# Kernel optimization log

Measured on AMD Instinct MI355X. Metric: run time of the kernel, lower is better.

Reference implementation:

```python
import jax, jax.numpy as jnp
import numpy as np

GAMMA = 1.0
EPS = 1e-8


def setup_inputs() -> dict:
    key = jax.random.key(0)
    k1, k2 = jax.random.split(key)
    inputs = jax.random.normal(k1, (16, 2048, 1024), dtype=jnp.float32)
    codebook = jax.random.normal(k2, (2048, 1024), dtype=jnp.float32)  # normal(1.0) init
    return {"inputs": inputs, "codebook": codebook}


def reference(inputs, codebook):
    # inputs: [B, T, D]; codebook: [K, D]
    features = jax.lax.stop_gradient(inputs)
    # similarity = sum over D of features[..., None, :] * codebook -> [B, T, K]
    similarity = jnp.einsum('btd,kd->btk', features, codebook)
    scores = jax.nn.softmax(similarity, axis=-1)  # [B, T, K]
    nn_idx = jnp.argmax(scores, axis=-1)  # [B, T]
    # one_hot(nn_idx) @ codebook == direct gather
    quantized = codebook[nn_idx]  # [B, T, D]
    quantized = quantized - jnp.mean(quantized, axis=-1, keepdims=True)
    quantized = quantized / jnp.linalg.norm(quantized, axis=-1, keepdims=True)
    # entropy loss
    flat = scores.reshape(-1, scores.shape[-1])  # [B*T, K]
    h_clust = -jnp.mean(jnp.sum(flat * jnp.log2(flat + EPS), axis=-1))
    diversity = jnp.mean(flat, axis=0)  # [K]
    h_diversity = -jnp.sum(diversity * jnp.log2(diversity + EPS))
    loss = h_clust - GAMMA * h_diversity
    quantization_loss = jnp.full(scores.shape, loss)  # [B, T, K], scalar broadcast
    # straight-through estimator
    quantized = inputs + jax.lax.stop_gradient(quantized - inputs)
    return (quantized, quantization_loss, nn_idx, codebook)
```

## Files before the change

kernel.cpp:

```cpp
#include <hip/hip_runtime.h>
#include <math.h>

#define M_TOTAL 32768
#define D_DIM   1024
#define K_DIM   2048

#define OUT0_OFF 0ULL
#define OUT1_OFF 33554432ULL
#define OUT2_OFF 100663296ULL
#define OUT3_OFF 100696064ULL

typedef _Float16 f16x4 __attribute__((ext_vector_type(4)));
typedef _Float16 f16x8 __attribute__((ext_vector_type(8)));
typedef float    f32x4 __attribute__((ext_vector_type(4)));

__device__ __forceinline__ void async_copy16(void* lds, const void* g) {
    __builtin_amdgcn_global_load_lds(
        (const __attribute__((address_space(1))) unsigned int*)g,
        (__attribute__((address_space(3))) unsigned int*)lds, 16, 0, 0);
}

__global__ __launch_bounds__(256) void convcb_kernel(const float* __restrict__ C,
                                                     _Float16* __restrict__ ch,
                                                     _Float16* __restrict__ cl) {
    const int i = blockIdx.x * 256 + threadIdx.x;
    const float4 c = ((const float4*)C)[i];
    f16x4 h, l;
    h.x = (_Float16)c.x; l.x = (_Float16)(c.x - (float)h.x);
    h.y = (_Float16)c.y; l.y = (_Float16)(c.y - (float)h.y);
    h.z = (_Float16)c.z; l.z = (_Float16)(c.z - (float)h.z);
    h.w = (_Float16)c.w; l.w = (_Float16)(c.w - (float)h.w);
    ((f16x4*)ch)[i] = h;
    ((f16x4*)cl)[i] = l;
}

__global__ __launch_bounds__(256) void gemm_kernel(const float* __restrict__ X,
                                                   const _Float16* __restrict__ CH,
                                                   const _Float16* __restrict__ CL,
                                                   float* __restrict__ S) {
    __shared__ _Float16 Ah[128 * 32];
    __shared__ _Float16 Bh[128 * 32];
    __shared__ _Float16 Bl[128 * 32];

    const int tid  = threadIdx.x;
    const int lane = tid & 63;
    const int wave = tid >> 6;
    const int n0 = blockIdx.x * 128;
    const int m0 = blockIdx.y * 128;
    const int wm = (wave & 1) * 64;
    const int wn = (wave >> 1) * 64;
    const int fr = lane & 15;
    const int fq = lane >> 4;

    f32x4 acc[4][4];
#pragma unroll
    for (int mi = 0; mi < 4; mi++)
#pragma unroll
        for (int ni = 0; ni < 4; ni++) {
            acc[mi][ni].x = 0.f; acc[mi][ni].y = 0.f;
            acc[mi][ni].z = 0.f; acc[mi][ni].w = 0.f;
        }

    for (int k0 = 0; k0 < D_DIM; k0 += 32) {
#pragma unroll
        for (int e = 0; e < 2; e++) {
            const int u   = wave * 128 + e * 64 + lane;
            const int row = u >> 2;
            const int off = u & 3;
            const size_t gofs = (size_t)(n0 + row) * D_DIM + k0 + off * 8;
            async_copy16((void*)(Bh + (size_t)(wave * 128 + e * 64) * 8), (const void*)(CH + gofs));
            async_copy16((void*)(Bl + (size_t)(wave * 128 + e * 64) * 8), (const void*)(CL + gofs));
        }
#pragma unroll
        for (int i = 0; i < 4; i++) {
            const int f = i * 256 + tid;
            const int r = f >> 3;
            const int q = f & 7;
            const float4 a = *(const float4*)(X + (size_t)(m0 + r) * D_DIM + k0 + q * 4);
            f16x4 h;
            h.x = (_Float16)a.x; h.y = (_Float16)a.y;
            h.z = (_Float16)a.z; h.w = (_Float16)a.w;
            *(f16x4*)(Ah + r * 32 + q * 4) = h;
        }
        __syncthreads();

        f16x8 afrag[4], bhfrag[4], blfrag[4];
#pragma unroll
        for (int t = 0; t < 4; t++) {
            afrag[t]  = *(const f16x8*)(Ah + (wm + t * 16 + fr) * 32 + fq * 8);
            bhfrag[t] = *(const f16x8*)(Bh + (wn + t * 16 + fr) * 32 + fq * 8);
            blfrag[t] = *(const f16x8*)(Bl + (wn + t * 16 + fr) * 32 + fq * 8);
        }
#pragma unroll
        for (int mi = 0; mi < 4; mi++)
#pragma unroll
            for (int ni = 0; ni < 4; ni++) {
                acc[mi][ni] = __builtin_amdgcn_mfma_f32_16x16x32_f16(afrag[mi], bhfrag[ni], acc[mi][ni], 0, 0, 0);
                acc[mi][ni] = __builtin_amdgcn_mfma_f32_16x16x32_f16(afrag[mi], blfrag[ni], acc[mi][ni], 0, 0, 0);
            }
        __syncthreads();
    }

#pragma unroll
    for (int mi = 0; mi < 4; mi++)
#pragma unroll
        for (int r = 0; r < 4; r++) {
            float* dst = S + (size_t)(m0 + wm + mi * 16 + fq * 4 + r) * K_DIM + n0 + wn;
#pragma unroll
            for (int ni = 0; ni < 4; ni++) dst[ni * 16 + fr] = acc[mi][ni][r];
        }
}

#define MARGIN 0.125f
__global__ __launch_bounds__(256) void rowstats_kernel(const float* __restrict__ S,
                                                       int* __restrict__ cnt,
                                                       int* __restrict__ cand,
                                                       float* __restrict__ div_acc,
                                                       float* __restrict__ hclust_acc) {
    __shared__ float sdiv[K_DIM];
    const int tid = threadIdx.x;
    for (int k = tid; k < K_DIM; k += 256) sdiv[k] = 0.0f;
    __syncthreads();

    const int lane = tid & 63;
    const int wave = tid >> 6;

    float dreg[32];
#pragma unroll
    for (int j = 0; j < 32; j++) dreg[j] = 0.0f;
    float ent_acc = 0.0f;

    for (int r8 = 0; r8 < 8; r8++) {
        const int row = blockIdx.x * 32 + wave * 8 + r8;
        const float* srow = S + (size_t)row * K_DIM;

        float v[32];
#pragma unroll
        for (int j = 0; j < 32; j++) v[j] = srow[lane + 64 * j];

        float m = v[0];
#pragma unroll
        for (int j = 1; j < 32; j++) m = fmaxf(m, v[j]);
        for (int off = 32; off > 0; off >>= 1) m = fmaxf(m, __shfl_xor(m, off, 64));

        const float thresh = m - MARGIN;
#pragma unroll
        for (int j = 0; j < 32; j++) {
            if (v[j] > thresh) {
                const int slot = atomicAdd(&cnt[row], 1);
                if (slot < 8) cand[row * 8 + slot] = lane + 64 * j;
            }
        }

        float Z = 0.0f;
#pragma unroll
        for (int j = 0; j < 32; j++) {
            v[j] = __expf(v[j] - m);
            Z += v[j];
        }
        for (int off = 32; off > 0; off >>= 1) Z += __shfl_xor(Z, off, 64);
        const float invZ = 1.0f / Z;

#pragma unroll
        for (int j = 0; j < 32; j++) {
            const float p = v[j] * invZ;
            dreg[j] += p;
            ent_acc += p * __log2f(p + 1e-8f);
        }
    }

#pragma unroll
    for (int j = 0; j < 32; j++) atomicAdd(&sdiv[lane + 64 * j], dreg[j]);
    for (int off = 32; off > 0; off >>= 1) ent_acc += __shfl_xor(ent_acc, off, 64);
    if (lane == 0) atomicAdd(hclust_acc, ent_acc);
    __syncthreads();

    for (int k = tid; k < K_DIM; k += 256) atomicAdd(&div_acc[k], sdiv[k]);
}

__global__ __launch_bounds__(256) void refine_kernel(const float* __restrict__ X,
                                                     const float* __restrict__ C,
                                                     const int* __restrict__ cnt,
                                                     const int* __restrict__ cand,
                                                     float* __restrict__ nn_out) {
    const int tid = threadIdx.x;
    const int lane = tid & 63;
    const int wave = tid >> 6;
    const int row = blockIdx.x * 4 + wave;

    const int n = min(cnt[row], 8);
    const float* x = X + (size_t)row * D_DIM;

    float4 xv[4];
#pragma unroll
    for (int q = 0; q < 4; q++) xv[q] = *(const float4*)(x + lane * 4 + 256 * q);

    double bestv = -1.0e300;
    int besti = 0x7fffffff;
    for (int c = 0; c < n; c++) {
        const int idx = cand[row * 8 + c];
        const float* cb = C + (size_t)idx * D_DIM;
        double s = 0.0;
#pragma unroll
        for (int q = 0; q < 4; q++) {
            const float4 cv = *(const float4*)(cb + lane * 4 + 256 * q);
            s += (double)xv[q].x * cv.x + (double)xv[q].y * cv.y +
                 (double)xv[q].z * cv.z + (double)xv[q].w * cv.w;
        }
        for (int off = 32; off > 0; off >>= 1) s += __shfl_xor(s, off, 64);
        if (s > bestv || (s == bestv && idx < besti)) { bestv = s; besti = idx; }
    }
    if (lane == 0) nn_out[row] = (float)besti;
}

__global__ __launch_bounds__(256) void finalize_kernel(const float* __restrict__ div_acc,
                                                       const float* __restrict__ hclust_acc,
                                                       float* __restrict__ loss_out) {
    __shared__ float red[256];
    const int tid = threadIdx.x;
    float sum = 0.0f;
    for (int k = tid; k < K_DIM; k += 256) {
        const float d = div_acc[k] * (1.0f / 32768.0f);
        sum += d * __log2f(d + 1e-8f);
    }
    red[tid] = sum;
    __syncthreads();
    for (int s = 128; s > 0; s >>= 1) {
        if (tid < s) red[tid] += red[tid + s];
        __syncthreads();
    }
    if (tid == 0) {
        const float h_clust = -hclust_acc[0] * (1.0f / 32768.0f);
        const float h_div = -red[0];
        loss_out[0] = h_clust - 1.0f * h_div;
    }
}

__global__ __launch_bounds__(256) void fill_kernel(float* __restrict__ out1,
                                                   const float* __restrict__ loss_ptr) {
    const float v = loss_ptr[0];
    const float4 f = make_float4(v, v, v, v);
    float4* o = (float4*)out1;
    const size_t stride = (size_t)gridDim.x * blockDim.x;
    for (size_t i = (size_t)blockIdx.x * blockDim.x + threadIdx.x; i < 16777216ULL; i += stride)
        o[i] = f;
}

__global__ __launch_bounds__(256) void quantize_kernel(const float* __restrict__ C,
                                                       const float* __restrict__ nn_f,
                                                       float* __restrict__ out0) {
    const int tid = threadIdx.x;
    const int lane = tid & 63;
    const int wave = tid >> 6;
    const int row = blockIdx.x * 4 + wave;

    const int idx = (int)nn_f[row];
    const float* c = C + (size_t)idx * D_DIM;

    float4 v[4];
    float sum = 0.0f;
#pragma unroll
    for (int q = 0; q < 4; q++) {
        v[q] = *(const float4*)(c + lane * 4 + 256 * q);
        sum += v[q].x + v[q].y + v[q].z + v[q].w;
    }
    for (int off = 32; off > 0; off >>= 1) sum += __shfl_xor(sum, off, 64);
    const float mean = sum * (1.0f / 1024.0f);

    float ss = 0.0f;
#pragma unroll
    for (int q = 0; q < 4; q++) {
        v[q].x -= mean; v[q].y -= mean; v[q].z -= mean; v[q].w -= mean;
        ss += v[q].x * v[q].x + v[q].y * v[q].y + v[q].z * v[q].z + v[q].w * v[q].w;
    }
    for (int off = 32; off > 0; off >>= 1) ss += __shfl_xor(ss, off, 64);
    const float inv = 1.0f / sqrtf(ss);

    float* o = out0 + (size_t)row * D_DIM;
#pragma unroll
    for (int q = 0; q < 4; q++) {
        float4 w = v[q];
        w.x *= inv; w.y *= inv; w.z *= inv; w.w *= inv;
        *(float4*)(o + lane * 4 + 256 * q) = w;
    }
}

__global__ __launch_bounds__(256) void copycb_kernel(const float* __restrict__ C,
                                                     float* __restrict__ out3) {
    const size_t i = (size_t)blockIdx.x * 256 + threadIdx.x;
    if (i < 524288ULL) ((float4*)out3)[i] = ((const float4*)C)[i];
}

extern "C" void kernel_launch(void* const* d_in, const int* in_sizes, int n_in,
                              void* d_out, int out_size, void* d_ws, size_t ws_size,
                              hipStream_t stream) {
    const float* X = (const float*)d_in[0];
    const float* C = (const float*)d_in[1];
    float* out = (float*)d_out;

    char* scratch = (char*)d_out;
    _Float16* CH  = (_Float16*)(scratch);
    _Float16* CL  = (_Float16*)(scratch + (4 << 20));
    int* cand     = (int*)(scratch + (8 << 20));
    int* cnt      = (int*)(scratch + (9 << 20));
    float* div_acc   = (float*)(scratch + (9 << 20) + (128 << 10));
    float* hclust    = div_acc + 2048;
    float* loss      = div_acc + 2049;

    float* S = out + OUT1_OFF;

    hipMemsetAsync(scratch + (9 << 20), 0, (128 << 10) + 8192 + 16, stream);

    convcb_kernel<<<2048, 256, 0, stream>>>(C, CH, CL);

    gemm_kernel<<<dim3(K_DIM / 128, M_TOTAL / 128), 256, 0, stream>>>(X, CH, CL, S);

    rowstats_kernel<<<M_TOTAL / 32, 256, 0, stream>>>(S, cnt, cand, div_acc, hclust);

    refine_kernel<<<M_TOTAL / 4, 256, 0, stream>>>(X, C, cnt, cand, out + OUT2_OFF);

    finalize_kernel<<<1, 256, 0, stream>>>(div_acc, hclust, loss);

    fill_kernel<<<8192, 256, 0, stream>>>(out + OUT1_OFF, loss);

    quantize_kernel<<<M_TOTAL / 4, 256, 0, stream>>>(C, out + OUT2_OFF, out + OUT0_OFF);

    copycb_kernel<<<2048, 256, 0, stream>>>(C, out + OUT3_OFF);
}
```

Before: 1.050 ms.

## Pre-convert X to fp16 and pipeline GEMM with double-buffered async LDS loads

Adds a separate pass that converts the inputs to fp16 so the GEMM can stream A through async global-to-LDS copies. The GEMM becomes a 256x128-tile, 512-thread kernel with double-buffered LDS, XOR-swizzled layout, XCD-aware block mapping and explicit vmcnt waits so loads overlap MFMA work. Rowstats reads are vectorised to float4, and the quantize step is fused into refine to avoid relaunching and rereading the index. Scratch is relocated into the out0/out3 regions; this costs an extra full pass over X and relies on hand-tuned wait counts being correct.

```diff
diff --git a/kernel.cpp b/kernel.cpp
--- a/kernel.cpp
+++ b/kernel.cpp
@@ -13,6 +13,10 @@
 typedef _Float16 f16x4 __attribute__((ext_vector_type(4)));
 typedef _Float16 f16x8 __attribute__((ext_vector_type(8)));
 typedef float    f32x4 __attribute__((ext_vector_type(4)));
+
+#define STR_(x) #x
+#define STR(x) STR_(x)
+#define WAITVM(N) asm volatile("s_waitcnt vmcnt(" STR(N) ")" ::: "memory")
 
 __device__ __forceinline__ void async_copy16(void* lds, const void* g) {
     __builtin_amdgcn_global_load_lds(
@@ -34,23 +38,101 @@
     ((f16x4*)cl)[i] = l;
 }
 
-__global__ __launch_bounds__(256) void gemm_kernel(const float* __restrict__ X,
+__global__ __launch_bounds__(256) void convx_kernel(const float* __restrict__ X,
+                                                    _Float16* __restrict__ xh) {
+    const size_t i = (size_t)blockIdx.x * 256 + threadIdx.x;
+    const float4 a = ((const float4*)X)[i];
+    f16x4 h;
+    h.x = (_Float16)a.x; h.y = (_Float16)a.y;
+    h.z = (_Float16)a.z; h.w = (_Float16)a.w;
+    ((f16x4*)xh)[i] = h;
+}
+
+__device__ __forceinline__ void loadA4(f16x8* a, const _Float16* Ab, int wm, int fr, int fq, int kh) {
+#pragma unroll
+    for (int mi = 0; mi < 4; mi++) {
+        const int row = wm + mi * 16 + fr;
+        a[mi] = *(const f16x8*)(Ab + kh * 8192 + row * 32 + (fq ^ (row & 3)) * 8);
+    }
+}
+__device__ __forceinline__ void loadB4(f16x8* b, const _Float16* Bb, int wn, int fr, int fq, int kh) {
+#pragma unroll
+    for (int ni = 0; ni < 4; ni++) {
+        const int row = wn + ni * 16 + fr;
+        b[ni] = *(const f16x8*)(Bb + kh * 4096 + row * 32 + (fq ^ (row & 3)) * 8);
+    }
+}
+
+__global__ __launch_bounds__(512) void gemm_kernel(const _Float16* __restrict__ XH,
                                                    const _Float16* __restrict__ CH,
                                                    const _Float16* __restrict__ CL,
                                                    float* __restrict__ S) {
-    __shared__ _Float16 Ah[128 * 32];
-    __shared__ _Float16 Bh[128 * 32];
-    __shared__ _Float16 Bl[128 * 32];
+    __shared__ _Float16 lds[65536];
+    _Float16* const A0  = lds;
+    _Float16* const Bh0 = lds + 16384;
+    _Float16* const Bl0 = lds + 24576;
+    _Float16* const A1  = lds + 32768;
+    _Float16* const Bh1 = lds + 49152;
+    _Float16* const Bl1 = lds + 57344;
 
     const int tid  = threadIdx.x;
     const int lane = tid & 63;
     const int wave = tid >> 6;
-    const int n0 = blockIdx.x * 128;
-    const int m0 = blockIdx.y * 128;
-    const int wm = (wave & 1) * 64;
-    const int wn = (wave >> 1) * 64;
+
+    const int bq  = blockIdx.x;
+    const int xcd = bq & 7;
+    const int idx = bq >> 3;
+    const int m0 = (xcd * 16 + (idx >> 4)) * 256;
+    const int n0 = (idx & 15) * 128;
+
+    const int wm = (wave & 3) * 64;
+    const int wn = (wave >> 2) * 64;
     const int fr = lane & 15;
     const int fq = lane >> 4;
+
+    size_t aoff[2][2]; int alds[2][2];
+#pragma unroll
+    for (int e = 0; e < 2; e++) {
+        const int U = (wave * 2 + e) * 64 + lane;
+        const int row = U >> 2;
+#pragma unroll
+        for (int kh = 0; kh < 2; kh++) {
+            aoff[e][kh] = (size_t)(m0 + row) * D_DIM + (size_t)(kh * 4 + ((U & 3) ^ (row & 3))) * 8;
+            alds[e][kh] = kh * 8192 + (wave * 2 + e) * 512;
+        }
+    }
+    size_t boff[2]; int blds[2];
+    {
+        const int U = wave * 64 + lane;
+        const int row = U >> 2;
+#pragma unroll
+        for (int kh = 0; kh < 2; kh++) {
+            boff[kh] = (size_t)(n0 + row) * D_DIM + (size_t)(kh * 4 + ((U & 3) ^ (row & 3))) * 8;
+            blds[kh] = kh * 4096 + wave * 512;
+        }
+    }
+
+#define STAGE_A(Abuf, KH, kb) do {                                                        \
+    async_copy16((void*)((Abuf) + alds[0][KH]), (const void*)(XH + aoff[0][KH] + (kb)));  \
+    async_copy16((void*)((Abuf) + alds[1][KH]), (const void*)(XH + aoff[1][KH] + (kb)));  \
+} while (0)
+#define STAGE_BH(Bbuf, KH, kb) async_copy16((void*)((Bbuf) + blds[KH]), (const void*)(CH + boff[KH] + (kb)))
+#define STAGE_BL(Bbuf, KH, kb) async_copy16((void*)((Bbuf) + blds[KH]), (const void*)(CL + boff[KH] + (kb)))
+
+#define PH_MFMA() do {                                                                    \
+    __builtin_amdgcn_s_barrier();                                                         \
+    asm volatile("s_waitcnt lgkmcnt(0)" ::: "memory");                                    \
+    __builtin_amdgcn_sched_barrier(0);                                                    \
+    __builtin_amdgcn_s_setprio(1);                                                        \
+    _Pragma("unroll")                                                                     \
+    for (int mi = 0; mi < 4; mi++) {                                                      \
+        _Pragma("unroll")                                                                 \
+        for (int ni = 0; ni < 4; ni++)                                                    \
+            acc[mi][ni] = __builtin_amdgcn_mfma_f32_16x16x32_f16(a[mi], b[ni], acc[mi][ni], 0, 0, 0); \
+    }                                                                                     \
+    __builtin_amdgcn_s_setprio(0);                                                        \
+    __builtin_amdgcn_s_barrier();                                                         \
+} while (0)
 
     f32x4 acc[4][4];
 #pragma unroll
@@ -61,45 +143,64 @@
             acc[mi][ni].z = 0.f; acc[mi][ni].w = 0.f;
         }
 
-    for (int k0 = 0; k0 < D_DIM; k0 += 32) {
-#pragma unroll
-        for (int e = 0; e < 2; e++) {
-            const int u   = wave * 128 + e * 64 + lane;
-            const int row = u >> 2;
-            const int off = u & 3;
-            const size_t gofs = (size_t)(n0 + row) * D_DIM + k0 + off * 8;
-            async_copy16((void*)(Bh + (size_t)(wave * 128 + e * 64) * 8), (const void*)(CH + gofs));
-            async_copy16((void*)(Bl + (size_t)(wave * 128 + e * 64) * 8), (const void*)(CL + gofs));
-        }
-#pragma unroll
-        for (int i = 0; i < 4; i++) {
-            const int f = i * 256 + tid;
-            const int r = f >> 3;
-            const int q = f & 7;
-            const float4 a = *(const float4*)(X + (size_t)(m0 + r) * D_DIM + k0 + q * 4);
-            f16x4 h;
-            h.x = (_Float16)a.x; h.y = (_Float16)a.y;
-            h.z = (_Float16)a.z; h.w = (_Float16)a.w;
-            *(f16x4*)(Ah + r * 32 + q * 4) = h;
-        }
-        __syncthreads();
-
-        f16x8 afrag[4], bhfrag[4], blfrag[4];
-#pragma unroll
-        for (int t = 0; t < 4; t++) {
-            afrag[t]  = *(const f16x8*)(Ah + (wm + t * 16 + fr) * 32 + fq * 8);
-            bhfrag[t] = *(const f16x8*)(Bh + (wn + t * 16 + fr) * 32 + fq * 8);
-            blfrag[t] = *(const f16x8*)(Bl + (wn + t * 16 + fr) * 32 + fq * 8);
-        }
-#pragma unroll
-        for (int mi = 0; mi < 4; mi++)
-#pragma unroll
-            for (int ni = 0; ni < 4; ni++) {
-                acc[mi][ni] = __builtin_amdgcn_mfma_f32_16x16x32_f16(afrag[mi], bhfrag[ni], acc[mi][ni], 0, 0, 0);
-                acc[mi][ni] = __builtin_amdgcn_mfma_f32_16x16x32_f16(afrag[mi], blfrag[ni], acc[mi][ni], 0, 0, 0);
-            }
-        __syncthreads();
-    }
+    f16x8 a[4], b[4];
+
+    STAGE_A(A0, 0, 0); STAGE_BH(Bh0, 0, 0);
+    STAGE_BL(Bl0, 0, 0);
+    STAGE_A(A0, 1, 0); STAGE_BH(Bh0, 1, 0);
+    STAGE_BL(Bl0, 1, 0);
+    WAITVM(5);
+    __builtin_amdgcn_s_barrier();
+
+    for (int t = 0; t < 15; t++) {
+        _Float16* const Ac  = (t & 1) ? A1 : A0;
+        _Float16* const Bhc = (t & 1) ? Bh1 : Bh0;
+        _Float16* const Blc = (t & 1) ? Bl1 : Bl0;
+        _Float16* const An  = (t & 1) ? A0 : A1;
+        _Float16* const Bhn = (t & 1) ? Bh0 : Bh1;
+        _Float16* const Bln = (t & 1) ? Bl0 : Bl1;
+        const size_t kb = (size_t)(t + 1) * 64;
+
+        loadA4(a, Ac, wm, fr, fq, 0);
+        loadB4(b, Bhc, wn, fr, fq, 0);
+        STAGE_A(An, 0, kb); STAGE_BH(Bhn, 0, kb);
+        WAITVM(7);
+        PH_MFMA();
+        loadB4(b, Blc, wn, fr, fq, 0);
+        STAGE_BL(Bln, 0, kb);
+        WAITVM(5);
+        PH_MFMA();
+        loadA4(a, Ac, wm, fr, fq, 1);
+        loadB4(b, Bhc, wn, fr, fq, 1);
+        STAGE_A(An, 1, kb); STAGE_BH(Bhn, 1, kb);
+        WAITVM(7);
+        PH_MFMA();
+        loadB4(b, Blc, wn, fr, fq, 1);
+        STAGE_BL(Bln, 1, kb);
+        WAITVM(5);
+        PH_MFMA();
+    }
+
+    loadA4(a, A1, wm, fr, fq, 0);
+    loadB4(b, Bh1, wn, fr, fq, 0);
+    WAITVM(4);
+    PH_MFMA();
+    loadB4(b, Bl1, wn, fr, fq, 0);
+    WAITVM(1);
+    PH_MFMA();
+    loadA4(a, A1, wm, fr, fq, 1);
+    loadB4(b, Bh1, wn, fr, fq, 1);
+    WAITVM(0);
+    PH_MFMA();
+    loadB4(b, Bl1, wn, fr, fq, 1);
+    __builtin_amdgcn_s_barrier();
+    asm volatile("s_waitcnt lgkmcnt(0)" ::: "memory");
+    __builtin_amdgcn_sched_barrier(0);
+#pragma unroll
+    for (int mi = 0; mi < 4; mi++)
+#pragma unroll
+        for (int ni = 0; ni < 4; ni++)
+            acc[mi][ni] = __builtin_amdgcn_mfma_f32_16x16x32_f16(a[mi], b[ni], acc[mi][ni], 0, 0, 0);
 
 #pragma unroll
     for (int mi = 0; mi < 4; mi++)
@@ -109,6 +210,10 @@
 #pragma unroll
             for (int ni = 0; ni < 4; ni++) dst[ni * 16 + fr] = acc[mi][ni][r];
         }
+#undef STAGE_A
+#undef STAGE_BH
+#undef STAGE_BL
+#undef PH_MFMA
 }
 
 #define MARGIN 0.125f
@@ -136,7 +241,11 @@
 
         float v[32];
 #pragma unroll
-        for (int j = 0; j < 32; j++) v[j] = srow[lane + 64 * j];
+        for (int q = 0; q < 8; q++) {
+            const float4 t4 = ((const float4*)srow)[q * 64 + lane];
+            v[q * 4 + 0] = t4.x; v[q * 4 + 1] = t4.y;
+            v[q * 4 + 2] = t4.z; v[q * 4 + 3] = t4.w;
+        }
 
         float m = v[0];
 #pragma unroll
@@ -148,7 +257,7 @@
         for (int j = 0; j < 32; j++) {
             if (v[j] > thresh) {
                 const int slot = atomicAdd(&cnt[row], 1);
-                if (slot < 8) cand[row * 8 + slot] = lane + 64 * j;
+                if (slot < 8) cand[row * 8 + slot] = (j >> 2) * 256 + lane * 4 + (j & 3);
             }
         }
 
@@ -170,7 +279,8 @@
     }
 
 #pragma unroll
-    for (int j = 0; j < 32; j++) atomicAdd(&sdiv[lane + 64 * j], dreg[j]);
+    for (int j = 0; j < 32; j++)
+        atomicAdd(&sdiv[(j >> 2) * 256 + lane * 4 + (j & 3)], dreg[j]);
     for (int off = 32; off > 0; off >>= 1) ent_acc += __shfl_xor(ent_acc, off, 64);
     if (lane == 0) atomicAdd(hclust_acc, ent_acc);
     __syncthreads();
@@ -178,11 +288,12 @@
     for (int k = tid; k < K_DIM; k += 256) atomicAdd(&div_acc[k], sdiv[k]);
 }
 
-__global__ __launch_bounds__(256) void refine_kernel(const float* __restrict__ X,
-                                                     const float* __restrict__ C,
-                                                     const int* __restrict__ cnt,
-                                                     const int* __restrict__ cand,
-                                                     float* __restrict__ nn_out) {
+__global__ __launch_bounds__(256) void refineq_kernel(const float* __restrict__ X,
+                                                      const float* __restrict__ C,
+                                                      const int* __restrict__ cnt,
+                                                      const int* __restrict__ cand,
+                                                      float* __restrict__ nn_out,
+                                                      float* __restrict__ out0) {
     const int tid = threadIdx.x;
     const int lane = tid & 63;
     const int wave = tid >> 6;
@@ -211,6 +322,34 @@
         if (s > bestv || (s == bestv && idx < besti)) { bestv = s; besti = idx; }
     }
     if (lane == 0) nn_out[row] = (float)besti;
+
+    const float* c = C + (size_t)besti * D_DIM;
+    float4 v[4];
+    float sum = 0.0f;
+#pragma unroll
+    for (int q = 0; q < 4; q++) {
+        v[q] = *(const float4*)(c + lane * 4 + 256 * q);
+        sum += v[q].x + v[q].y + v[q].z + v[q].w;
+    }
+    for (int off = 32; off > 0; off >>= 1) sum += __shfl_xor(sum, off, 64);
+    const float mean = sum * (1.0f / 1024.0f);
+
+    float ss = 0.0f;
+#pragma unroll
+    for (int q = 0; q < 4; q++) {
+        v[q].x -= mean; v[q].y -= mean; v[q].z -= mean; v[q].w -= mean;
+        ss += v[q].x * v[q].x + v[q].y * v[q].y + v[q].z * v[q].z + v[q].w * v[q].w;
+    }
+    for (int off = 32; off > 0; off >>= 1) ss += __shfl_xor(ss, off, 64);
+    const float inv = 1.0f / sqrtf(ss);
+
+    float* o = out0 + (size_t)row * D_DIM;
+#pragma unroll
+    for (int q = 0; q < 4; q++) {
+        float4 w = v[q];
+        w.x *= inv; w.y *= inv; w.z *= inv; w.w *= inv;
+        *(float4*)(o + lane * 4 + 256 * q) = w;
+    }
 }
 
 __global__ __launch_bounds__(256) void finalize_kernel(const float* __restrict__ div_acc,
@@ -246,45 +385,6 @@
         o[i] = f;
 }
 
-__global__ __launch_bounds__(256) void quantize_kernel(const float* __restrict__ C,
-                                                       const float* __restrict__ nn_f,
-                                                       float* __restrict__ out0) {
-    const int tid = threadIdx.x;
-    const int lane = tid & 63;
-    const int wave = tid >> 6;
-    const int row = blockIdx.x * 4 + wave;
-
-    const int idx = (int)nn_f[row];
-    const float* c = C + (size_t)idx * D_DIM;
-
-    float4 v[4];
-    float sum = 0.0f;
-#pragma unroll
-    for (int q = 0; q < 4; q++) {
-        v[q] = *(const float4*)(c + lane * 4 + 256 * q);
-        sum += v[q].x + v[q].y + v[q].z + v[q].w;
-    }
-    for (int off = 32; off > 0; off >>= 1) sum += __shfl_xor(sum, off, 64);
-    const float mean = sum * (1.0f / 1024.0f);
-
-    float ss = 0.0f;
-#pragma unroll
-    for (int q = 0; q < 4; q++) {
-        v[q].x -= mean; v[q].y -= mean; v[q].z -= mean; v[q].w -= mean;
-        ss += v[q].x * v[q].x + v[q].y * v[q].y + v[q].z * v[q].z + v[q].w * v[q].w;
-    }
-    for (int off = 32; off > 0; off >>= 1) ss += __shfl_xor(ss, off, 64);
-    const float inv = 1.0f / sqrtf(ss);
-
-    float* o = out0 + (size_t)row * D_DIM;
-#pragma unroll
-    for (int q = 0; q < 4; q++) {
-        float4 w = v[q];
-        w.x *= inv; w.y *= inv; w.z *= inv; w.w *= inv;
-        *(float4*)(o + lane * 4 + 256 * q) = w;
-    }
-}
-
 __global__ __launch_bounds__(256) void copycb_kernel(const float* __restrict__ C,
                                                      float* __restrict__ out3) {
     const size_t i = (size_t)blockIdx.x * 256 + threadIdx.x;
@@ -301,29 +401,33 @@
     char* scratch = (char*)d_out;
     _Float16* CH  = (_Float16*)(scratch);
     _Float16* CL  = (_Float16*)(scratch + (4 << 20));
-    int* cand     = (int*)(scratch + (8 << 20));
-    int* cnt      = (int*)(scratch + (9 << 20));
-    float* div_acc   = (float*)(scratch + (9 << 20) + (128 << 10));
-    float* hclust    = div_acc + 2048;
-    float* loss      = div_acc + 2049;
+    _Float16* XH  = (_Float16*)(scratch + (16 << 20));
+
+    char* s3 = (char*)(out + OUT3_OFF);
+    int* cand      = (int*)s3;
+    int* cnt       = (int*)(s3 + (1 << 20));
+    float* div_acc = (float*)(s3 + (1 << 20) + (128 << 10));
+    float* hclust  = div_acc + 2048;
+    float* loss    = div_acc + 2049;
 
     float* S = out + OUT1_OFF;
 
-    hipMemsetAsync(scratch + (9 << 20), 0, (128 << 10) + 8192 + 16, stream);
+    hipMemsetAsync(s3 + (1 << 20), 0, (128 << 10) + 8192 + 16, stream);
 
     convcb_kernel<<<2048, 256, 0, stream>>>(C, CH, CL);
 
-    gemm_kernel<<<dim3(K_DIM / 128, M_TOTAL / 128), 256, 0, stream>>>(X, CH, CL, S);
+    convx_kernel<<<32768, 256, 0, stream>>>(X, XH);
+
+    gemm_kernel<<<2048, 512, 0, stream>>>(XH, CH, CL, S);
 
     rowstats_kernel<<<M_TOTAL / 32, 256, 0, stream>>>(S, cnt, cand, div_acc, hclust);
 
-    refine_kernel<<<M_TOTAL / 4, 256, 0, stream>>>(X, C, cnt, cand, out + OUT2_OFF);
+    refineq_kernel<<<M_TOTAL / 4, 256, 0, stream>>>(X, C, cnt, cand,
+                                                    out + OUT2_OFF, out + OUT0_OFF);
 
     finalize_kernel<<<1, 256, 0, stream>>>(div_acc, hclust, loss);
 
     fill_kernel<<<8192, 256, 0, stream>>>(out + OUT1_OFF, loss);
 
-    quantize_kernel<<<M_TOTAL / 4, 256, 0, stream>>>(C, out + OUT2_OFF, out + OUT0_OFF);
-
     copycb_kernel<<<2048, 256, 0, stream>>>(C, out + OUT3_OFF);
 }
```

Result: faster. 958.9 us (-8.7%).
